# Kernel tuning notes

Hardware: AMD Instinct MI355X
Metric: run time of the kernel (lower is better)

The kernel has to match this reference:

```python
import jax, jax.numpy as jnp
import numpy as np

B, T, C, H, W = 16, 8, 3, 14, 14
HID, IND, N = 32, 16, 3
HW = H * W

def _conv(x, w, b):
    # NCHW conv, 3x3, SAME padding (stride 1)
    y = jax.lax.conv_general_dilated(x, w, (1, 1), 'SAME',
                                     dimension_numbers=('NCHW', 'OIHW', 'NCHW'))
    return y + b[None, :, None, None]

def _maxpool3(x):
    # MaxPool2d(kernel=3, stride=1, padding=1) -> same spatial size
    return jax.lax.reduce_window(x, -jnp.inf, jax.lax.max,
                                 (1, 1, 3, 3), (1, 1, 1, 1),
                                 [(0, 0), (0, 0), (1, 1), (1, 1)])

def _cell(x, h, td, wg, bgn, wc, bcn):
    # ConvGRU cell with additive top-down modulation on the gate input
    comb = jnp.concatenate([x, h], axis=1)
    if td is not None:
        comb = comb + td
    r, z = jnp.split(jax.nn.sigmoid(_conv(comb, wg, bgn)), 2, axis=1)
    cand = jnp.tanh(_conv(jnp.concatenate([x, r * h], axis=1), wc, bcn))
    return (1.0 - z) * h + z * cand

def _forward(x, Wg, bg, Wc, bc,
             bu_w0, bu_b0, bu_w1, bu_b1, bu_w2, bu_b2,
             td_w0, td_b0, td_w1, td_b1,
             fc1_w, fc1_b, fc2_w, fc2_b):
    bu_w = [bu_w0, bu_w1, bu_w2]
    bu_b = [bu_b0, bu_b1, bu_b2]
    td_w = [td_w0, td_w1]
    td_b = [td_b0, td_b1]
    hidden = [jnp.zeros((B, HID, H, W), x.dtype) for _ in range(N)]
    for t in range(T + N - 1):
        # torch aliases hidden_states_prev = hidden_states after t=0;
        # at t=0 the prev list is a separate all-zeros list.
        src = [jnp.zeros_like(h) for h in hidden] if t == 0 else hidden
        for node in range(N):
            if node == 0:
                if t >= T:  # no in-nodes and input exhausted -> skip (empty bottomup)
                    continue
                bu = x[:, t].reshape(B, -1)
            else:
                if t == 0:  # upstream hidden is all-zeros -> count_nonzero==0 -> skip
                    continue
                bu = _maxpool3(src[node - 1]).reshape(B, -1)
            bu = (bu @ bu_w[node].T + bu_b[node]).reshape(B, IND, H, W)
            td = None
            if node < N - 1 and t >= 2:  # downstream hidden nonzero from t>=2
                m = _maxpool3(src[node + 1]).reshape(B, -1)
                td = (m @ td_w[node].T + td_b[node]).reshape(B, IND + HID, H, W)
            hidden[node] = _cell(bu, hidden[node], td,
                                 Wg[node], bg[node], Wc[node], bc[node])
    p = jax.nn.relu(hidden[N - 1].reshape(B, -1))
    p = jax.nn.relu(p @ fc1_w.T + fc1_b)
    return p @ fc2_w.T + fc2_b

def setup_inputs() -> dict:
    key = jax.random.key(0)
    ks = jax.random.split(key, 16)
    s = 0.02
    inp = {}
    inp['x'] = jax.random.normal(ks[0], (B, T, C, H, W), jnp.float32)
    inp['Wg'] = jax.random.normal(ks[1], (N, 2 * HID, IND + HID, 3, 3), jnp.float32) * s
    inp['bg'] = jnp.zeros((N, 2 * HID), jnp.float32)
    inp['Wc'] = jax.random.normal(ks[2], (N, HID, IND + HID, 3, 3), jnp.float32) * s
    inp['bc'] = jnp.zeros((N, HID), jnp.float32)
    inp['bu_w0'] = jax.random.normal(ks[3], (IND * HW, C * HW), jnp.float32) * s
    inp['bu_b0'] = jnp.zeros((IND * HW,), jnp.float32)
    inp['bu_w1'] = jax.random.normal(ks[4], (IND * HW, HID * HW), jnp.float32) * s
    inp['bu_b1'] = jnp.zeros((IND * HW,), jnp.float32)
    inp['bu_w2'] = jax.random.normal(ks[5], (IND * HW, HID * HW), jnp.float32) * s
    inp['bu_b2'] = jnp.zeros((IND * HW,), jnp.float32)
    inp['td_w0'] = jax.random.normal(ks[6], ((IND + HID) * HW, HID * HW), jnp.float32) * s
    inp['td_b0'] = jnp.zeros(((IND + HID) * HW,), jnp.float32)
    inp['td_w1'] = jax.random.normal(ks[7], ((IND + HID) * HW, HID * HW), jnp.float32) * s
    inp['td_b1'] = jnp.zeros(((IND + HID) * HW,), jnp.float32)
    inp['fc1_w'] = jax.random.normal(ks[8], (100, HID * HW), jnp.float32) * s
    inp['fc1_b'] = jnp.zeros((100,), jnp.float32)
    inp['fc2_w'] = jax.random.normal(ks[9], (10, 100), jnp.float32) * s
    inp['fc2_b'] = jnp.zeros((10,), jnp.float32)
    return inp

def reference(x, Wg, bg, Wc, bc, bu_w0, bu_b0, bu_w1, bu_b1, bu_w2, bu_b2, td_w0, td_b0, td_w1, td_b1, fc1_w, fc1_b, fc2_w, fc2_b):
    return _forward(x, Wg, bg, Wc, bc, bu_w0, bu_b0, bu_w1, bu_b1, bu_w2, bu_b2, td_w0, td_b0, td_w1, td_b1, fc1_w, fc1_b, fc2_w, fc2_b)
```

## Files before the change

### kernel.cpp

```cpp
#include <hip/hip_runtime.h>
#include <math.h>


__global__ __launch_bounds__(256) void gemv16(
    const float* __restrict__ act, int act_stride,
    const float* __restrict__ W,
    float* __restrict__ partial, int N, int K, int KSLICE, int S)
{
    const int wave = threadIdx.x >> 6;
    const int lane = threadIdx.x & 63;
    const int n0   = (blockIdx.x << 6) + (wave << 4);
    const int s    = blockIdx.y;
    const int kb   = s * KSLICE;
    const int len  = min(KSLICE, K - kb);
    const int off  = lane << 3;
    const bool g0  = (off + 4) <= len;
    const bool g1  = (off + 8) <= len;
    const float4 z4 = make_float4(0.f, 0.f, 0.f, 0.f);

    float4 a0[16], a1[16];
#pragma unroll
    for (int b = 0; b < 16; ++b) {
        const float* ap = act + b * act_stride + kb + off;
        a0[b] = g0 ? *(const float4*)(ap)     : z4;
        a1[b] = g1 ? *(const float4*)(ap + 4) : z4;
    }

    const float* wp = W + (size_t)n0 * K + kb + off;
    float4 w0 = g0 ? *(const float4*)(wp)     : z4;
    float4 w1 = g1 ? *(const float4*)(wp + 4) : z4;

    for (int r = 0; r < 16; ++r) {
        float4 nw0 = z4, nw1 = z4;
        if (r < 15) {
            const float* np = wp + (size_t)(r + 1) * K;
            nw0 = g0 ? *(const float4*)(np)     : z4;
            nw1 = g1 ? *(const float4*)(np + 4) : z4;
        }
        float t[16];
#pragma unroll
        for (int b = 0; b < 16; ++b) {
            float v;
            v = w0.x * a0[b].x;
            v = fmaf(w0.y, a0[b].y, v);
            v = fmaf(w0.z, a0[b].z, v);
            v = fmaf(w0.w, a0[b].w, v);
            v = fmaf(w1.x, a1[b].x, v);
            v = fmaf(w1.y, a1[b].y, v);
            v = fmaf(w1.z, a1[b].z, v);
            v = fmaf(w1.w, a1[b].w, v);
            t[b] = v;
        }
#pragma unroll
        for (int m = 1; m < 64; m <<= 1) {
#pragma unroll
            for (int b = 0; b < 16; ++b) t[b] += __shfl_xor(t[b], m, 64);
        }
        if (lane == 0) {
            float* pp = partial + ((size_t)(n0 + r) * 16) * S + s;
#pragma unroll
            for (int b = 0; b < 16; ++b) pp[(size_t)b * S] = t[b];
        }
        w0 = nw0; w1 = nw1;
    }
}

__global__ __launch_bounds__(256) void reduce_partial(
    const float* __restrict__ partial, const float* __restrict__ bias,
    float* __restrict__ out, int N, int S)
{
    const int i = blockIdx.x * 256 + threadIdx.x;
    if (i >= N * 16) return;
    const int n = i >> 4, bb = i & 15;
    const float* p = partial + (size_t)i * S;
    float v = bias[n];
    for (int s = 0; s < S; ++s) v += p[s];
    out[bb * N + n] = v;
}

__global__ __launch_bounds__(256) void copy_x_pad(
    const float* __restrict__ x, float* __restrict__ dst, int t)
{
    int i = blockIdx.x * 256 + threadIdx.x;
    if (i >= 16 * 592) return;
    int b = i / 592, k = i - b * 592;
    dst[i] = (k < 588) ? x[b * 4704 + t * 588 + k] : 0.f;
}

__global__ __launch_bounds__(256) void maxpool3_k(const float* __restrict__ h,
                                                  float* __restrict__ out)
{
    int i = blockIdx.x * 256 + threadIdx.x;
    if (i >= 16 * 32 * 196) return;
    int p = i % 196;
    int y = p / 14, x = p - y * 14;
    const float* base = h + (i - p);
    int y0 = max(y - 1, 0), y1 = min(y + 1, 13);
    int x0 = max(x - 1, 0), x1 = min(x + 1, 13);
    float m = -INFINITY;
    for (int yy = y0; yy <= y1; ++yy)
        for (int xc = x0; xc <= x1; ++xc)
            m = fmaxf(m, base[yy * 14 + xc]);
    out[i] = m;
}

template<bool HAS_TD>
__global__ __launch_bounds__(256) void gate_conv(
    const float* __restrict__ bu, const float* __restrict__ h,
    const float* __restrict__ td,
    const float* __restrict__ Wg, const float* __restrict__ bg,
    float* __restrict__ rh, float* __restrict__ z)
{
    int i = blockIdx.x * 256 + threadIdx.x;
    if (i >= 16 * 64 * 196) return;
    int p = i % 196;
    int rest = i / 196;
    int o = rest & 63;
    int b = rest >> 6;
    int y = p / 14, x = p - y * 14;
    int ky0 = (y == 0) ? 1 : 0, ky1 = (y == 13) ? 2 : 3;
    int kx0 = (x == 0) ? 1 : 0, kx1 = (x == 13) ? 2 : 3;

    float acc = bg[o];
    const float* wb  = Wg + o * 432;
    const float* bub = bu + b * 3136;
    const float* hb  = h  + b * 6272;
    const float* tdb = HAS_TD ? td + b * 9408 : nullptr;

    for (int ci = 0; ci < 48; ++ci) {
        const float* src = (ci < 16) ? (bub + ci * 196) : (hb + (ci - 16) * 196);
        const float* w   = wb + ci * 9;
        const float* tp  = HAS_TD ? (tdb + ci * 196) : nullptr;
        for (int ky = ky0; ky < ky1; ++ky) {
            int q = p + (ky - 1) * 14 - 1;
            for (int kx = kx0; kx < kx1; ++kx) {
                float v = src[q + kx];
                if (HAS_TD) v += tp[q + kx];
                acc += v * w[ky * 3 + kx];
            }
        }
    }
    float g = 1.f / (1.f + expf(-acc));
    if (o < 32) {
        int idx = (b * 32 + o) * 196 + p;
        rh[idx] = g * h[idx];
    } else {
        int idx = (b * 32 + (o - 32)) * 196 + p;
        z[idx] = g;
    }
}

__global__ __launch_bounds__(256) void cand_conv(
    const float* __restrict__ bu, const float* __restrict__ rh,
    const float* __restrict__ z,
    const float* __restrict__ Wc, const float* __restrict__ bc,
    float* __restrict__ h)
{
    int i = blockIdx.x * 256 + threadIdx.x;
    if (i >= 16 * 32 * 196) return;
    int p = i % 196;
    int rest = i / 196;
    int o = rest & 31;
    int b = rest >> 5;
    int y = p / 14, x = p - y * 14;
    int ky0 = (y == 0) ? 1 : 0, ky1 = (y == 13) ? 2 : 3;
    int kx0 = (x == 0) ? 1 : 0, kx1 = (x == 13) ? 2 : 3;

    float acc = bc[o];
    const float* wb  = Wc + o * 432;
    const float* bub = bu + b * 3136;
    const float* rhb = rh + b * 6272;

    for (int ci = 0; ci < 48; ++ci) {
        const float* src = (ci < 16) ? (bub + ci * 196) : (rhb + (ci - 16) * 196);
        const float* w   = wb + ci * 9;
        for (int ky = ky0; ky < ky1; ++ky) {
            int q = p + (ky - 1) * 14 - 1;
            for (int kx = kx0; kx < kx1; ++kx)
                acc += src[q + kx] * w[ky * 3 + kx];
        }
    }
    float cand = tanhf(acc);
    int idx = (b * 32 + o) * 196 + p;
    float zv = z[idx];
    h[idx] = (1.f - zv) * h[idx] + zv * cand;
}

template<bool RELU_IN, bool RELU_OUT>
__global__ __launch_bounds__(256) void matmul_tn(
    const float* __restrict__ in, int in_stride,
    const float* __restrict__ W, const float* __restrict__ bias,
    float* __restrict__ out, int N, int K)
{
    __shared__ float lds[16 * 512];
    const int tid  = threadIdx.x;
    const int wave = tid >> 6;
    const int lane = tid & 63;
    const int n0   = blockIdx.x * 16 + wave * 4;

    bool rv[4];
    const float* wr[4];
#pragma unroll
    for (int r = 0; r < 4; ++r) {
        rv[r] = (n0 + r) < N;
        wr[r] = W + (size_t)(n0 + r) * K;
    }

    float acc[4][16];
#pragma unroll
    for (int r = 0; r < 4; ++r)
#pragma unroll
        for (int b = 0; b < 16; ++b) acc[r][b] = 0.f;

    for (int k0 = 0; k0 < K; k0 += 512) {
        const int len = min(512, K - k0);
        __syncthreads();
        for (int i = tid; i < 16 * 512; i += 256) {
            const int b = i >> 9, kk = i & 511;
            if (kk < len) {
                float v = in[b * in_stride + k0 + kk];
                if (RELU_IN) v = fmaxf(v, 0.f);
                lds[i] = v;
            }
        }
        __syncthreads();
        for (int kk = lane * 4; kk < len; kk += 256) {
            float4 w[4];
#pragma unroll
            for (int r = 0; r < 4; ++r)
                w[r] = rv[r] ? *(const float4*)(wr[r] + k0 + kk)
                             : make_float4(0.f, 0.f, 0.f, 0.f);
#pragma unroll
            for (int b = 0; b < 16; ++b) {
                const float4 v = *(const float4*)(&lds[(b << 9) + kk]);
#pragma unroll
                for (int r = 0; r < 4; ++r) {
                    acc[r][b] += w[r].x * v.x + w[r].y * v.y +
                                 w[r].z * v.z + w[r].w * v.w;
                }
            }
        }
    }

#pragma unroll
    for (int r = 0; r < 4; ++r) {
        const float brv = rv[r] ? bias[n0 + r] : 0.f;
#pragma unroll
        for (int b = 0; b < 16; ++b) {
            float v = acc[r][b];
#pragma unroll
            for (int o = 32; o > 0; o >>= 1)
                v += __shfl_down(v, o, 64);
            if (lane == 0 && rv[r]) {
                v += brv;
                if (RELU_OUT) v = fmaxf(v, 0.f);
                out[b * N + (n0 + r)] = v;
            }
        }
    }
}

extern "C" void kernel_launch(void* const* d_in, const int* in_sizes, int n_in,
                              void* d_out, int out_size, void* d_ws, size_t ws_size,
                              hipStream_t stream)
{
    (void)in_sizes; (void)n_in; (void)out_size; (void)ws_size;

    const float* x     = (const float*)d_in[0];
    const float* Wg    = (const float*)d_in[1];
    const float* bg    = (const float*)d_in[2];
    const float* Wc    = (const float*)d_in[3];
    const float* bc    = (const float*)d_in[4];
    const float* bu_w[3] = {(const float*)d_in[5], (const float*)d_in[7], (const float*)d_in[9]};
    const float* bu_b[3] = {(const float*)d_in[6], (const float*)d_in[8], (const float*)d_in[10]};
    const float* td_w[2] = {(const float*)d_in[11], (const float*)d_in[13]};
    const float* td_b[2] = {(const float*)d_in[12], (const float*)d_in[14]};
    const float* fc1_w = (const float*)d_in[15];
    const float* fc1_b = (const float*)d_in[16];
    const float* fc2_w = (const float*)d_in[17];
    const float* fc2_b = (const float*)d_in[18];
    float* out = (float*)d_out;

    float* ws     = (float*)d_ws;
    float* hid0   = ws;
    float* hid1   = hid0 + 100352;
    float* hid2   = hid1 + 100352;
    float* bu_buf = hid2 + 100352;
    float* td_buf = bu_buf + 50176;
    float* rh_buf = td_buf + 150528;
    float* z_buf  = rh_buf + 100352;
    float* p1_buf = z_buf + 100352;
    float* xpad   = p1_buf + 1600;
    float* mpA    = xpad + 9472;
    float* mpB    = mpA + 100352;
    float* mpC    = mpB + 100352;
    float* part   = mpC + 100352;

    hipMemsetAsync(ws, 0, 3 * 100352 * sizeof(float), stream);

    auto TD = [&](const float* mp, const float* Wp, const float* bp) {
        gemv16<<<dim3(147, 13), 256, 0, stream>>>(mp, 6272, Wp, part, 9408, 6272, 512, 13);
        reduce_partial<<<588, 256, 0, stream>>>(part, bp, td_buf, 9408, 13);
    };
    auto BU = [&](const float* mp, const float* Wp, const float* bp) {
        gemv16<<<dim3(49, 13), 256, 0, stream>>>(mp, 6272, Wp, part, 3136, 6272, 512, 13);
        reduce_partial<<<196, 256, 0, stream>>>(part, bp, bu_buf, 3136, 13);
    };

    for (int t = 0; t < 10; ++t) {
        if (t < 8) {
            copy_x_pad<<<37, 256, 0, stream>>>(x, xpad, t);
            gemv16<<<dim3(49, 8), 256, 0, stream>>>(xpad, 592, bu_w[0], part, 3136, 588, 80, 8);
            reduce_partial<<<196, 256, 0, stream>>>(part, bu_b[0], bu_buf, 3136, 8);
            if (t >= 2) {
                TD(mpB, td_w[0], td_b[0]);
                gate_conv<true><<<784, 256, 0, stream>>>(bu_buf, hid0, td_buf, Wg, bg, rh_buf, z_buf);
            } else {
                gate_conv<false><<<784, 256, 0, stream>>>(bu_buf, hid0, nullptr, Wg, bg, rh_buf, z_buf);
            }
            cand_conv<<<392, 256, 0, stream>>>(bu_buf, rh_buf, z_buf, Wc, bc, hid0);
        }
        if (t >= 1) {
            if (t < 8) maxpool3_k<<<392, 256, 0, stream>>>(hid0, mpA);
            BU(mpA, bu_w[1], bu_b[1]);
            const float* wg1 = Wg + 27648;
            const float* bg1 = bg + 64;
            if (t >= 2) {
                maxpool3_k<<<392, 256, 0, stream>>>(hid2, mpC);
                TD(mpC, td_w[1], td_b[1]);
                gate_conv<true><<<784, 256, 0, stream>>>(bu_buf, hid1, td_buf, wg1, bg1, rh_buf, z_buf);
            } else {
                gate_conv<false><<<784, 256, 0, stream>>>(bu_buf, hid1, nullptr, wg1, bg1, rh_buf, z_buf);
            }
            cand_conv<<<392, 256, 0, stream>>>(bu_buf, rh_buf, z_buf, Wc + 13824, bc + 32, hid1);
        }
        if (t >= 1) {
            maxpool3_k<<<392, 256, 0, stream>>>(hid1, mpB);
            BU(mpB, bu_w[2], bu_b[2]);
            gate_conv<false><<<784, 256, 0, stream>>>(bu_buf, hid2, nullptr,
                                                      Wg + 2 * 27648, bg + 128, rh_buf, z_buf);
            cand_conv<<<392, 256, 0, stream>>>(bu_buf, rh_buf, z_buf, Wc + 2 * 13824, bc + 64, hid2);
        }
    }

    matmul_tn<true, true><<<dim3(7), dim3(256), 0, stream>>>(hid2, 6272, fc1_w, fc1_b, p1_buf, 100, 6272);
    matmul_tn<false, false><<<dim3(1), dim3(256), 0, stream>>>(p1_buf, 100, fc2_w, fc2_b, out, 10, 100);
}
```

Baseline: 8.967 ms.

## Replace split-K GEMV plus reduce with full-K shared-memory tiled GEMV

Swaps the split-K gemv16 kernel and its separate reduce_partial pass for a single gemv_full kernel. Each block stages 16-row activation chunks in double-buffered LDS and loops over all of K, so each wave accumulates 4 output rows for 16 batch items and writes the final result with the bias added. This removes the partial-sum buffer, the extra reduction launches and the copy_x_pad kernel, since x is now read directly through a stride. In exchange there is far less parallelism along K (588 or 196 blocks with no K split), and each output still needs a full 64-lane shuffle reduction.

```diff
diff --git a/kernel.cpp b/kernel.cpp
--- a/kernel.cpp
+++ b/kernel.cpp
@@ -2,89 +2,82 @@
 #include <math.h>
 
 
-__global__ __launch_bounds__(256) void gemv16(
+#define GEMV_CHUNK 256
+
+__global__ __launch_bounds__(256) void gemv_full(
     const float* __restrict__ act, int act_stride,
-    const float* __restrict__ W,
-    float* __restrict__ partial, int N, int K, int KSLICE, int S)
-{
-    const int wave = threadIdx.x >> 6;
-    const int lane = threadIdx.x & 63;
-    const int n0   = (blockIdx.x << 6) + (wave << 4);
-    const int s    = blockIdx.y;
-    const int kb   = s * KSLICE;
-    const int len  = min(KSLICE, K - kb);
-    const int off  = lane << 3;
-    const bool g0  = (off + 4) <= len;
-    const bool g1  = (off + 8) <= len;
+    const float* __restrict__ W, const float* __restrict__ bias,
+    float* __restrict__ out, int N, int K)
+{
+    __shared__ float lact[2][16 * GEMV_CHUNK];
+    const int tid  = threadIdx.x;
+    const int wave = tid >> 6;
+    const int lane = tid & 63;
+    const int n0   = blockIdx.x * 16 + wave * 4;
+    const int off  = lane << 2;
     const float4 z4 = make_float4(0.f, 0.f, 0.f, 0.f);
 
-    float4 a0[16], a1[16];
-#pragma unroll
-    for (int b = 0; b < 16; ++b) {
-        const float* ap = act + b * act_stride + kb + off;
-        a0[b] = g0 ? *(const float4*)(ap)     : z4;
-        a1[b] = g1 ? *(const float4*)(ap + 4) : z4;
-    }
-
-    const float* wp = W + (size_t)n0 * K + kb + off;
-    float4 w0 = g0 ? *(const float4*)(wp)     : z4;
-    float4 w1 = g1 ? *(const float4*)(wp + 4) : z4;
-
-    for (int r = 0; r < 16; ++r) {
-        float4 nw0 = z4, nw1 = z4;
-        if (r < 15) {
-            const float* np = wp + (size_t)(r + 1) * K;
-            nw0 = g0 ? *(const float4*)(np)     : z4;
-            nw1 = g1 ? *(const float4*)(np + 4) : z4;
-        }
-        float t[16];
+    float acc[4][16];
+#pragma unroll
+    for (int r = 0; r < 4; ++r)
+#pragma unroll
+        for (int b = 0; b < 16; ++b) acc[r][b] = 0.f;
+
+    const float* wr0 = W + (size_t)n0 * K;
+
+    int p = 0;
+    for (int kb = 0; kb < K; kb += GEMV_CHUNK) {
+        const int len = min(GEMV_CHUNK, K - kb);
+
+#pragma unroll
+        for (int pass = 0; pass < 4; ++pass) {
+            const int i = (pass << 10) + (tid << 2);
+            const int b = i >> 8, k = i & 255;
+            float4 v = (k < len)
+                ? *(const float4*)(act + (size_t)b * act_stride + kb + k) : z4;
+            *(float4*)&lact[p][i] = v;
+        }
+
+        const bool g = off < len;
+        float4 w[4];
+#pragma unroll
+        for (int r = 0; r < 4; ++r)
+            w[r] = g ? *(const float4*)(wr0 + (size_t)r * K + kb + off) : z4;
+
+        __syncthreads();
+
+#pragma unroll
+        for (int h2 = 0; h2 < 2; ++h2) {
+            float4 la[8];
+#pragma unroll
+            for (int b = 0; b < 8; ++b)
+                la[b] = *(const float4*)&lact[p][((h2 * 8 + b) << 8) + off];
+#pragma unroll
+            for (int r = 0; r < 4; ++r)
+#pragma unroll
+                for (int b = 0; b < 8; ++b) {
+                    float v = acc[r][h2 * 8 + b];
+                    v = fmaf(w[r].x, la[b].x, v);
+                    v = fmaf(w[r].y, la[b].y, v);
+                    v = fmaf(w[r].z, la[b].z, v);
+                    v = fmaf(w[r].w, la[b].w, v);
+                    acc[r][h2 * 8 + b] = v;
+                }
+        }
+        p ^= 1;
+    }
+
+#pragma unroll
+    for (int r = 0; r < 4; ++r) {
+        const float bv = bias[n0 + r];
 #pragma unroll
         for (int b = 0; b < 16; ++b) {
-            float v;
-            v = w0.x * a0[b].x;
-            v = fmaf(w0.y, a0[b].y, v);
-            v = fmaf(w0.z, a0[b].z, v);
-            v = fmaf(w0.w, a0[b].w, v);
-            v = fmaf(w1.x, a1[b].x, v);
-            v = fmaf(w1.y, a1[b].y, v);
-            v = fmaf(w1.z, a1[b].z, v);
-            v = fmaf(w1.w, a1[b].w, v);
-            t[b] = v;
-        }
-#pragma unroll
-        for (int m = 1; m < 64; m <<= 1) {
-#pragma unroll
-            for (int b = 0; b < 16; ++b) t[b] += __shfl_xor(t[b], m, 64);
-        }
-        if (lane == 0) {
-            float* pp = partial + ((size_t)(n0 + r) * 16) * S + s;
-#pragma unroll
-            for (int b = 0; b < 16; ++b) pp[(size_t)b * S] = t[b];
-        }
-        w0 = nw0; w1 = nw1;
-    }
-}
-
-__global__ __launch_bounds__(256) void reduce_partial(
-    const float* __restrict__ partial, const float* __restrict__ bias,
-    float* __restrict__ out, int N, int S)
-{
-    const int i = blockIdx.x * 256 + threadIdx.x;
-    if (i >= N * 16) return;
-    const int n = i >> 4, bb = i & 15;
-    const float* p = partial + (size_t)i * S;
-    float v = bias[n];
-    for (int s = 0; s < S; ++s) v += p[s];
-    out[bb * N + n] = v;
-}
-
-__global__ __launch_bounds__(256) void copy_x_pad(
-    const float* __restrict__ x, float* __restrict__ dst, int t)
-{
-    int i = blockIdx.x * 256 + threadIdx.x;
-    if (i >= 16 * 592) return;
-    int b = i / 592, k = i - b * 592;
-    dst[i] = (k < 588) ? x[b * 4704 + t * 588 + k] : 0.f;
+            float v = acc[r][b];
+#pragma unroll
+            for (int m = 1; m < 64; m <<= 1) v += __shfl_xor(v, m, 64);
+            if (lane == 0) out[(size_t)b * N + n0 + r] = v + bv;
+        }
+    }
 }
 
 __global__ __launch_bounds__(256) void maxpool3_k(const float* __restrict__ h,
@@ -290,28 +283,23 @@
     float* rh_buf = td_buf + 150528;
     float* z_buf  = rh_buf + 100352;
     float* p1_buf = z_buf + 100352;
-    float* xpad   = p1_buf + 1600;
-    float* mpA    = xpad + 9472;
+    float* mpA    = p1_buf + 1600;
     float* mpB    = mpA + 100352;
     float* mpC    = mpB + 100352;
-    float* part   = mpC + 100352;
 
     hipMemsetAsync(ws, 0, 3 * 100352 * sizeof(float), stream);
 
     auto TD = [&](const float* mp, const float* Wp, const float* bp) {
-        gemv16<<<dim3(147, 13), 256, 0, stream>>>(mp, 6272, Wp, part, 9408, 6272, 512, 13);
-        reduce_partial<<<588, 256, 0, stream>>>(part, bp, td_buf, 9408, 13);
+        gemv_full<<<588, 256, 0, stream>>>(mp, 6272, Wp, bp, td_buf, 9408, 6272);
     };
     auto BU = [&](const float* mp, const float* Wp, const float* bp) {
-        gemv16<<<dim3(49, 13), 256, 0, stream>>>(mp, 6272, Wp, part, 3136, 6272, 512, 13);
-        reduce_partial<<<196, 256, 0, stream>>>(part, bp, bu_buf, 3136, 13);
+        gemv_full<<<196, 256, 0, stream>>>(mp, 6272, Wp, bp, bu_buf, 3136, 6272);
     };
 
     for (int t = 0; t < 10; ++t) {
         if (t < 8) {
-            copy_x_pad<<<37, 256, 0, stream>>>(x, xpad, t);
-            gemv16<<<dim3(49, 8), 256, 0, stream>>>(xpad, 592, bu_w[0], part, 3136, 588, 80, 8);
-            reduce_partial<<<196, 256, 0, stream>>>(part, bu_b[0], bu_buf, 3136, 8);
+            gemv_full<<<196, 256, 0, stream>>>(x + t * 588, 4704, bu_w[0], bu_b[0],
+                                               bu_buf, 3136, 588);
             if (t >= 2) {
                 TD(mpB, td_w[0], td_b[0]);
                 gate_conv<true><<<784, 256, 0, stream>>>(bu_buf, hid0, td_buf, Wg, bg, rh_buf, z_buf);
```

After: 7.781 ms. 13.2% less time.
